# Kernel optimization log

Measured on AMD Instinct MI355X. Metric: run time of the kernel, lower is better.

Reference implementation:

```python
import jax, jax.numpy as jnp
import numpy as np

N = 50000   # nodes
E = 800000  # edges
IN = 128
HID = 128
L = 4       # GraphConv layers
OUT = 47    # classes
EPS = 1e-5  # BatchNorm eps


def setup_inputs() -> dict:
    key = jax.random.key(0)
    ks = jax.random.split(key, 12)
    feat = jax.random.normal(ks[0], (N, IN), jnp.float32)
    src = jax.random.randint(ks[1], (E,), 0, N, jnp.int32)
    dst = jax.random.randint(ks[2], (E,), 0, N, jnp.int32)
    enc_W = jax.random.normal(ks[3], (L, IN, HID), jnp.float32) * 0.05
    enc_bias = jnp.zeros((HID,), jnp.float32)
    bn_gamma = jnp.ones((L, HID), jnp.float32)
    bn_beta = jnp.zeros((L, HID), jnp.float32)
    bn_mean = jax.random.normal(ks[4], (L, HID), jnp.float32) * 0.1
    bn_var = jnp.ones((L, HID), jnp.float32) + 0.1 * jax.random.uniform(ks[5], (L, HID), jnp.float32)
    cls_W0 = jax.random.normal(ks[6], (HID * L, HID), jnp.float32) * 0.05
    cls_b0 = jnp.zeros((HID,), jnp.float32)
    cls_gamma0 = jnp.ones((HID,), jnp.float32)
    cls_beta0 = jnp.zeros((HID,), jnp.float32)
    cls_mean0 = jax.random.normal(ks[7], (HID,), jnp.float32) * 0.1
    cls_var0 = jnp.ones((HID,), jnp.float32) + 0.1 * jax.random.uniform(ks[8], (HID,), jnp.float32)
    cls_W1 = jax.random.normal(ks[9], (HID, OUT), jnp.float32) * 0.05
    cls_b1 = jnp.zeros((OUT,), jnp.float32)
    return dict(feat=feat, src=src, dst=dst, enc_W=enc_W, enc_bias=enc_bias,
                bn_gamma=bn_gamma, bn_beta=bn_beta, bn_mean=bn_mean, bn_var=bn_var,
                cls_W0=cls_W0, cls_b0=cls_b0, cls_gamma0=cls_gamma0, cls_beta0=cls_beta0,
                cls_mean0=cls_mean0, cls_var0=cls_var0, cls_W1=cls_W1, cls_b1=cls_b1)


def _bn_eval(x, gamma, beta, mean, var):
    return (x - mean) * (gamma * jax.lax.rsqrt(var + EPS)) + beta


def reference(feat, src, dst, enc_W, enc_bias, bn_gamma, bn_beta, bn_mean, bn_var,
              cls_W0, cls_b0, cls_gamma0, cls_beta0, cls_mean0, cls_var0, cls_W1, cls_b1):
    ones = jnp.ones((E,), jnp.float32)
    out_deg = jnp.clip(jax.ops.segment_sum(ones, src, num_segments=N), 1.0)
    in_deg = jnp.clip(jax.ops.segment_sum(ones, dst, num_segments=N), 1.0)
    norm_src = jax.lax.rsqrt(out_deg)[:, None]  # [N,1]
    norm_dst = jax.lax.rsqrt(in_deg)[:, None]

    h = feat  # inference: dropout = identity
    feat_lst = []
    for i in range(L):
        # GraphConv 'both': D_out^{-1/2} pre-scale, XW, scatter-add over edges, D_in^{-1/2} post-scale
        hw = (h * norm_src) @ enc_W[i]                         # [N,HID]
        agg = jax.ops.segment_sum(hw[src], dst, num_segments=N)  # sparse neighbor aggregation
        h = agg * norm_dst
        if i == L - 1:  # only last GraphConv has bias
            h = h + enc_bias
        h = _bn_eval(h, bn_gamma[i], bn_beta[i], bn_mean[i], bn_var[i])
        h = jax.nn.relu(h)
        feat_lst.append(h)

    h = jnp.concatenate(feat_lst, axis=-1)  # JK concat -> [N, HID*L]
    # classifier layer 0: Linear + BN + ReLU (dropout off in eval)
    h = _bn_eval(h @ cls_W0 + cls_b0, cls_gamma0, cls_beta0, cls_mean0, cls_var0)
    h = jax.nn.relu(h)
    # classifier layer 1: Linear only
    return h @ cls_W1 + cls_b1  # [N, OUT]
```

## Files before the change

kernel.cpp:

```cpp
#include <hip/hip_runtime.h>
#include <hip/hip_bf16.h>
#include <hip/hip_fp16.h>

#define EPS 1e-5f
#define HB 128
#define HRANGE 25600
#define NN2 51200

typedef __attribute__((ext_vector_type(8))) short short8;
typedef __attribute__((ext_vector_type(4))) float f32x4;

__device__ __forceinline__ unsigned short f2bf_rn(float f) {
    unsigned u = __builtin_bit_cast(unsigned, f);
    u += 0x7fffu + ((u >> 16) & 1u);
    return (unsigned short)(u >> 16);
}
__device__ __forceinline__ float bf2f(unsigned short h) {
    return __builtin_bit_cast(float, (unsigned)h << 16);
}
__device__ __forceinline__ unsigned packsplit(float x) {
    unsigned short h = f2bf_rn(x);
    unsigned short l = f2bf_rn(x - bf2f(h));
    return ((unsigned)h << 16) | l;
}

__global__ __launch_bounds__(1024) void hist_kernel(
    const int* __restrict__ src, const int* __restrict__ dst,
    unsigned* __restrict__ histW, int E, int EperB) {
    __shared__ unsigned cnt[HRANGE];
    const int b = blockIdx.x, tid = threadIdx.x;
    const long e0 = (long)b * EperB;
    const long e1 = min(e0 + (long)EperB, (long)E);
    #pragma unroll 2
    for (int arr = 0; arr < 2; ++arr) {
        const int* a = arr ? src : dst;
        for (int j = tid; j < HRANGE; j += 1024) cnt[j] = 0;
        __syncthreads();
        for (long e = e0 + tid; e < e1; e += 1024) {
            int v = a[e];
            atomicAdd(&cnt[v >> 1], 1u << ((v & 1) << 4));
        }
        __syncthreads();
        unsigned* o = histW + ((size_t)(arr * HB + b)) * HRANGE;
        for (int j = tid; j < HRANGE; j += 1024) o[j] = cnt[j];
        __syncthreads();
    }
}

__global__ __launch_bounds__(256) void merge_kernel(
    const unsigned short* __restrict__ hist16, int* __restrict__ indeg,
    unsigned short* __restrict__ bp16, float* __restrict__ nsrc,
    float* __restrict__ ndst, int N) {
    int n = blockIdx.x * blockDim.x + threadIdx.x;
    if (n >= NN2) return;
    unsigned s = 0;
    #pragma unroll 8
    for (int b = 0; b < HB; ++b) {
        unsigned c = hist16[(size_t)b * NN2 + n];
        bp16[(size_t)b * NN2 + n] = (unsigned short)s;
        s += c;
    }
    unsigned s2 = 0;
    #pragma unroll 8
    for (int b = 0; b < HB; ++b) s2 += hist16[(size_t)(HB + b) * NN2 + n];
    if (n < N) {
        indeg[n] = (int)s;
        ndst[n] = rsqrtf((float)max((int)s, 1));
        nsrc[n] = rsqrtf((float)max((int)s2, 1));
    }
}

__global__ __launch_bounds__(256) void scan_partial_kernel(const int* __restrict__ deg,
                                                           int* __restrict__ bsums, int n) {
    __shared__ int wsum[4];
    const int tid = threadIdx.x, lane = tid & 63, wid = tid >> 6;
    const int i0 = blockIdx.x * 1024 + tid * 4;
    int s = 0;
    if (i0 + 3 < n) {
        int4 v = *(const int4*)(deg + i0);
        s = v.x + v.y + v.z + v.w;
    } else {
        for (int j = 0; j < 4; ++j) if (i0 + j < n) s += deg[i0 + j];
    }
    #pragma unroll
    for (int off = 32; off >= 1; off >>= 1) s += __shfl_down(s, off, 64);
    if (lane == 0) wsum[wid] = s;
    __syncthreads();
    if (tid == 0) bsums[blockIdx.x] = wsum[0] + wsum[1] + wsum[2] + wsum[3];
}

__global__ __launch_bounds__(64) void scan_bsums_kernel(int* __restrict__ bsums,
                                                        int* __restrict__ offs, int nb, int n) {
    int lane = threadIdx.x;
    int v = (lane < nb) ? bsums[lane] : 0;
    int x = v;
    #pragma unroll
    for (int off = 1; off < 64; off <<= 1) {
        int t = __shfl_up(x, off, 64);
        if (lane >= off) x += t;
    }
    if (lane < nb) bsums[lane] = x - v;
    if (lane == 63) offs[n] = x;
}

__global__ __launch_bounds__(256) void scan_final_kernel(const int* __restrict__ deg,
                                                         const int* __restrict__ bsums,
                                                         int* __restrict__ offs, int n) {
    __shared__ int wsum[4];
    const int tid = threadIdx.x, lane = tid & 63, wid = tid >> 6;
    const int i0 = blockIdx.x * 1024 + tid * 4;
    int d0 = 0, d1 = 0, d2 = 0, d3 = 0;
    if (i0 + 3 < n) {
        int4 v = *(const int4*)(deg + i0);
        d0 = v.x; d1 = v.y; d2 = v.z; d3 = v.w;
    } else {
        if (i0 + 0 < n) d0 = deg[i0 + 0];
        if (i0 + 1 < n) d1 = deg[i0 + 1];
        if (i0 + 2 < n) d2 = deg[i0 + 2];
        if (i0 + 3 < n) d3 = deg[i0 + 3];
    }
    int s = d0 + d1 + d2 + d3;
    int x = s;
    #pragma unroll
    for (int off = 1; off < 64; off <<= 1) {
        int t = __shfl_up(x, off, 64);
        if (lane >= off) x += t;
    }
    if (lane == 63) wsum[wid] = x;
    __syncthreads();
    int wpre = 0;
    #pragma unroll
    for (int w = 0; w < 4; ++w) if (w < wid) wpre += wsum[w];
    int base = bsums[blockIdx.x] + wpre + (x - s);
    if (i0 + 0 < n) offs[i0 + 0] = base;
    if (i0 + 1 < n) offs[i0 + 1] = base + d0;
    if (i0 + 2 < n) offs[i0 + 2] = base + d0 + d1;
    if (i0 + 3 < n) offs[i0 + 3] = base + d0 + d1 + d2;
}

__global__ __launch_bounds__(1024) void fill_kernel(
    const int* __restrict__ src, const int* __restrict__ dst,
    const int* __restrict__ offs, const unsigned short* __restrict__ bp16,
    int* __restrict__ csc, int E, int EperB) {
    __shared__ unsigned cur[HRANGE];
    const int b = blockIdx.x, tid = threadIdx.x;
    const long e0 = (long)b * EperB;
    const long e1 = min(e0 + (long)EperB, (long)E);
    for (int j = tid; j < HRANGE; j += 1024) cur[j] = 0;
    __syncthreads();
    const unsigned short* bprow = bp16 + (size_t)b * NN2;
    for (long e = e0 + tid; e < e1; e += 1024) {
        int d = dst[e];
        int sh = (d & 1) << 4;
        unsigned old = atomicAdd(&cur[d >> 1], 1u << sh);
        unsigned rank = (old >> sh) & 0xffffu;
        unsigned p = (unsigned)offs[d] + (unsigned)bprow[d] + rank;
        csc[p] = src[e];
    }
}

__global__ void pack_w_kernel(const float* __restrict__ B, short* __restrict__ hi,
                              short* __restrict__ lo, int K, int NCF,
                              int strideB, int ncols) {
    int t = blockIdx.x * blockDim.x + threadIdx.x;
    int KF = K >> 5;
    int total = NCF * KF * 64;
    if (t >= total) return;
    int lane = t & 63;
    int kf = (t >> 6) % KF;
    int cf = (t >> 6) / KF;
    int col = cf * 16 + (lane & 15);
    int k0 = kf * 32 + (lane >> 4) * 8;
    int o = t * 8;
    #pragma unroll
    for (int j = 0; j < 8; ++j) {
        float x = (col < ncols) ? B[(size_t)(k0 + j) * strideB + col] : 0.f;
        unsigned short h = f2bf_rn(x);
        hi[o + j] = (short)h;
        lo[o + j] = (short)f2bf_rn(x - bf2f(h));
    }
}

template<bool PACKED>
__global__ __launch_bounds__(256) void mfma_gemm_kernel(
    const void* __restrict__ Av, const short* __restrict__ Bhi, const short* __restrict__ Blo,
    const float* __restrict__ nsrc, __half* __restrict__ C, int M) {
    __shared__ short Bh_sh[16384];
    __shared__ short Bl_sh[16384];
    const int tid = threadIdx.x;
    const int lane = tid & 63;
    const int wid  = tid >> 6;
    const int row0 = blockIdx.x * 128 + wid * 32;
    const int rsub = lane & 15;
    const int kg   = lane >> 4;

    short8 ahi[2][4], alo[2][4];
    #pragma unroll
    for (int rf = 0; rf < 2; ++rf) {
        const int rowa = min(row0 + rf * 16 + rsub, M - 1);
        #pragma unroll
        for (int kf = 0; kf < 4; ++kf) {
            short8 h, l;
            if (PACKED) {
                const unsigned* ap = (const unsigned*)Av + (size_t)rowa * 128 + kg * 8;
                uint4 u0 = *(const uint4*)(ap + kf * 32);
                uint4 u1 = *(const uint4*)(ap + kf * 32 + 4);
                unsigned uu[8] = {u0.x, u0.y, u0.z, u0.w, u1.x, u1.y, u1.z, u1.w};
                #pragma unroll
                for (int j = 0; j < 8; ++j) {
                    h[j] = (short)(uu[j] >> 16);
                    l[j] = (short)(uu[j] & 0xffffu);
                }
            } else {
                const float* ap = (const float*)Av + (size_t)rowa * 128 + kg * 8;
                float4 v0 = *(const float4*)(ap + kf * 32);
                float4 v1 = *(const float4*)(ap + kf * 32 + 4);
                float v[8] = {v0.x, v0.y, v0.z, v0.w, v1.x, v1.y, v1.z, v1.w};
                #pragma unroll
                for (int j = 0; j < 8; ++j) {
                    unsigned short hb = f2bf_rn(v[j]);
                    h[j] = (short)hb;
                    l[j] = (short)f2bf_rn(v[j] - bf2f(hb));
                }
            }
            ahi[rf][kf] = h; alo[rf][kf] = l;
        }
    }

    #pragma unroll
    for (int i = 0; i < 8; ++i) {
        int o = (tid + i * 256) * 8;
        *(uint4*)&Bh_sh[o] = *(const uint4*)&Bhi[o];
        *(uint4*)&Bl_sh[o] = *(const uint4*)&Blo[o];
    }
    __syncthreads();

    f32x4 acc[2][8];
    #pragma unroll
    for (int rf = 0; rf < 2; ++rf)
        #pragma unroll
        for (int cf = 0; cf < 8; ++cf) acc[rf][cf] = (f32x4){0.f, 0.f, 0.f, 0.f};

    #pragma unroll
    for (int cf = 0; cf < 8; ++cf) {
        #pragma unroll
        for (int kf = 0; kf < 4; ++kf) {
            int o = ((cf * 4 + kf) * 64 + lane) * 8;
            short8 bh = *(const short8*)&Bh_sh[o];
            short8 bl = *(const short8*)&Bl_sh[o];
            #pragma unroll
            for (int rf = 0; rf < 2; ++rf) {
                acc[rf][cf] = __builtin_amdgcn_mfma_f32_16x16x32_bf16(ahi[rf][kf], bh, acc[rf][cf], 0, 0, 0);
                acc[rf][cf] = __builtin_amdgcn_mfma_f32_16x16x32_bf16(alo[rf][kf], bh, acc[rf][cf], 0, 0, 0);
                acc[rf][cf] = __builtin_amdgcn_mfma_f32_16x16x32_bf16(ahi[rf][kf], bl, acc[rf][cf], 0, 0, 0);
            }
        }
    }

    #pragma unroll
    for (int rf = 0; rf < 2; ++rf)
        #pragma unroll
        for (int r = 0; r < 4; ++r) {
            int row = row0 + rf * 16 + kg * 4 + r;
            if (row < M) {
                float sc = nsrc[row];
                __half* cp = C + (size_t)row * 128 + rsub;
                #pragma unroll
                for (int cf = 0; cf < 8; ++cf) cp[cf * 16] = __float2half(acc[rf][cf][r] * sc);
            }
        }
}

__global__ __launch_bounds__(256) void aggregate_kernel(
    const __half* __restrict__ hw, const int* __restrict__ offs, const int* __restrict__ csc,
    const float* __restrict__ norm_dst, const float* __restrict__ bias,
    const float* __restrict__ gamma, const float* __restrict__ beta,
    const float* __restrict__ mean, const float* __restrict__ var,
    unsigned* __restrict__ hout, int n) {
    const int lane = threadIdx.x & 63;
    const int gw = (blockIdx.x * blockDim.x + threadIdx.x) >> 6;
    const int nw = (gridDim.x * blockDim.x) >> 6;
    const int c = lane * 2;

    const float sc0 = gamma[c] * rsqrtf(var[c] + EPS);
    const float sc1 = gamma[c + 1] * rsqrtf(var[c + 1] + EPS);
    const float mn0 = mean[c], mn1 = mean[c + 1];
    const float bt0 = beta[c], bt1 = beta[c + 1];
    const float bi0 = bias ? bias[c] : 0.f;
    const float bi1 = bias ? bias[c + 1] : 0.f;

    for (int v = gw; v < n; v += nw) {
        int e0 = offs[v], e1 = offs[v + 1];
        float2 acc = make_float2(0.f, 0.f);
        int e = e0;
        for (; e + 4 <= e1; e += 4) {
            int s0 = csc[e], s1 = csc[e + 1], s2 = csc[e + 2], s3 = csc[e + 3];
            float2 p0 = __half22float2(*(const __half2*)(hw + (size_t)s0 * 128 + c));
            float2 p1 = __half22float2(*(const __half2*)(hw + (size_t)s1 * 128 + c));
            float2 p2 = __half22float2(*(const __half2*)(hw + (size_t)s2 * 128 + c));
            float2 p3 = __half22float2(*(const __half2*)(hw + (size_t)s3 * 128 + c));
            acc.x += (p0.x + p1.x) + (p2.x + p3.x);
            acc.y += (p0.y + p1.y) + (p2.y + p3.y);
        }
        for (; e < e1; ++e) {
            int s0 = csc[e];
            float2 p0 = __half22float2(*(const __half2*)(hw + (size_t)s0 * 128 + c));
            acc.x += p0.x; acc.y += p0.y;
        }
        float nd = norm_dst[v];
        float h0 = fmaxf((acc.x * nd + bi0 - mn0) * sc0 + bt0, 0.f);
        float h1 = fmaxf((acc.y * nd + bi1 - mn1) * sc1 + bt1, 0.f);
        uint2 w = make_uint2(packsplit(h0), packsplit(h1));
        *(uint2*)(hout + (size_t)v * 128 + c) = w;
    }
}

__global__ __launch_bounds__(256) void classifier_kernel(
    const unsigned* __restrict__ h1, const unsigned* __restrict__ h2,
    const unsigned* __restrict__ h3, const unsigned* __restrict__ h4,
    const short* __restrict__ Bhi, const short* __restrict__ Blo,
    const short* __restrict__ W1hi, const short* __restrict__ W1lo,
    const float* __restrict__ b0,
    const float* __restrict__ g, const float* __restrict__ bt,
    const float* __restrict__ mn, const float* __restrict__ vr,
    const float* __restrict__ b1,
    float* __restrict__ out, int M) {
    __shared__ short Bh_sh[2][4096];
    __shared__ short Bl_sh[2][4096];
    __shared__ unsigned zw[4][16 * 128];
    const int tid = threadIdx.x, lane = tid & 63, wid = tid >> 6;
    const int rsub = lane & 15;
    const int kg   = lane >> 4;
    const int row0 = blockIdx.x * 128 + wid * 32;
    const unsigned* hb[4] = {h1, h2, h3, h4};

    const int scf = tid >> 5, ssub = tid & 31;
    const int sl = scf * 512 + ssub * 16;

    float biasv[8], scalev[8], meanv[8], betav[8];
    #pragma unroll
    for (int cf = 0; cf < 8; ++cf) {
        int col = cf * 16 + rsub;
        biasv[cf] = b0[col];
        scalev[cf] = g[col] * rsqrtf(vr[col] + EPS);
        meanv[cf] = mn[col];
        betav[cf] = bt[col];
    }

    f32x4 acc[2][8];
    #pragma unroll
    for (int rf = 0; rf < 2; ++rf)
        #pragma unroll
        for (int cf = 0; cf < 8; ++cf) acc[rf][cf] = (f32x4){0.f, 0.f, 0.f, 0.f};

    {
        size_t goff = ((size_t)(scf * 16 + 0) * 64) * 8 + ssub * 16;
        *(uint4*)&Bh_sh[0][sl]     = *(const uint4*)&Bhi[goff];
        *(uint4*)&Bh_sh[0][sl + 8] = *(const uint4*)&Bhi[goff + 8];
        *(uint4*)&Bl_sh[0][sl]     = *(const uint4*)&Blo[goff];
        *(uint4*)&Bl_sh[0][sl + 8] = *(const uint4*)&Blo[goff + 8];
    }
    __syncthreads();

    const int rowa0 = min(row0 + rsub, M - 1);
    const int rowa1 = min(row0 + 16 + rsub, M - 1);

    for (int kf16 = 0; kf16 < 16; ++kf16) {
        const int cur = kf16 & 1;
        uint4 st0, st1, st2, st3;
        if (kf16 < 15) {
            size_t goff = ((size_t)(scf * 16 + kf16 + 1) * 64) * 8 + ssub * 16;
            st0 = *(const uint4*)&Bhi[goff];
            st1 = *(const uint4*)&Bhi[goff + 8];
            st2 = *(const uint4*)&Blo[goff];
            st3 = *(const uint4*)&Blo[goff + 8];
        }
        short8 ah[2], al[2];
        #pragma unroll
        for (int rf = 0; rf < 2; ++rf) {
            const unsigned* ap = hb[kf16 >> 2] + (size_t)(rf ? rowa1 : rowa0) * 128
                                 + (kf16 & 3) * 32 + kg * 8;
            uint4 u0 = *(const uint4*)(ap);
            uint4 u1 = *(const uint4*)(ap + 4);
            unsigned uu[8] = {u0.x, u0.y, u0.z, u0.w, u1.x, u1.y, u1.z, u1.w};
            #pragma unroll
            for (int j = 0; j < 8; ++j) {
                ah[rf][j] = (short)(uu[j] >> 16);
                al[rf][j] = (short)(uu[j] & 0xffffu);
            }
        }
        #pragma unroll
        for (int cf = 0; cf < 8; ++cf) {
            int o = (cf * 64 + lane) * 8;
            short8 bh = *(const short8*)&Bh_sh[cur][o];
            short8 bl = *(const short8*)&Bl_sh[cur][o];
            #pragma unroll
            for (int rf = 0; rf < 2; ++rf) {
                acc[rf][cf] = __builtin_amdgcn_mfma_f32_16x16x32_bf16(ah[rf], bh, acc[rf][cf], 0, 0, 0);
                acc[rf][cf] = __builtin_amdgcn_mfma_f32_16x16x32_bf16(al[rf], bh, acc[rf][cf], 0, 0, 0);
                acc[rf][cf] = __builtin_amdgcn_mfma_f32_16x16x32_bf16(ah[rf], bl, acc[rf][cf], 0, 0, 0);
            }
        }
        if (kf16 < 15) {
            *(uint4*)&Bh_sh[cur ^ 1][sl]     = st0;
            *(uint4*)&Bh_sh[cur ^ 1][sl + 8] = st1;
            *(uint4*)&Bl_sh[cur ^ 1][sl]     = st2;
            *(uint4*)&Bl_sh[cur ^ 1][sl + 8] = st3;
        }
        __syncthreads();
    }

    f32x4 oacc[2][3];
    #pragma unroll
    for (int rf = 0; rf < 2; ++rf)
        #pragma unroll
        for (int cf = 0; cf < 3; ++cf) oacc[rf][cf] = (f32x4){0.f, 0.f, 0.f, 0.f};

    #pragma unroll
    for (int rf = 0; rf < 2; ++rf) {
        #pragma unroll
        for (int cf = 0; cf < 8; ++cf) {
            int col = cf * 16 + rsub;
            #pragma unroll
            for (int r = 0; r < 4; ++r) {
                int rloc = kg * 4 + r;
                float z = fmaxf((acc[rf][cf][r] + biasv[cf] - meanv[cf]) * scalev[cf] + betav[cf], 0.f);
                zw[wid][rloc * 128 + (col ^ ((rloc & 7) << 2))] = packsplit(z);
            }
        }
        const int rloc = rsub;
        const int sw = (rloc & 7) << 2;
        #pragma unroll
        for (int kf = 0; kf < 4; ++kf) {
            int k0 = kf * 32 + kg * 8;
            uint4 ua = *(const uint4*)&zw[wid][rloc * 128 + (k0 ^ sw)];
            uint4 ub = *(const uint4*)&zw[wid][rloc * 128 + ((k0 + 4) ^ sw)];
            unsigned uu[8] = {ua.x, ua.y, ua.z, ua.w, ub.x, ub.y, ub.z, ub.w};
            short8 zh, zl;
            #pragma unroll
            for (int j = 0; j < 8; ++j) {
                zh[j] = (short)(uu[j] >> 16);
                zl[j] = (short)(uu[j] & 0xffffu);
            }
            #pragma unroll
            for (int cf = 0; cf < 3; ++cf) {
                int bidx = ((cf * 4 + kf) * 64 + lane) * 8;
                short8 wh = *(const short8*)(W1hi + bidx);
                short8 wl = *(const short8*)(W1lo + bidx);
                oacc[rf][cf] = __builtin_amdgcn_mfma_f32_16x16x32_bf16(zh, wh, oacc[rf][cf], 0, 0, 0);
                oacc[rf][cf] = __builtin_amdgcn_mfma_f32_16x16x32_bf16(zl, wh, oacc[rf][cf], 0, 0, 0);
                oacc[rf][cf] = __builtin_amdgcn_mfma_f32_16x16x32_bf16(zh, wl, oacc[rf][cf], 0, 0, 0);
            }
        }
    }

    #pragma unroll
    for (int rf = 0; rf < 2; ++rf)
        #pragma unroll
        for (int cf = 0; cf < 3; ++cf) {
            int col = cf * 16 + rsub;
            if (col < 47) {
                float bb = b1[col];
                #pragma unroll
                for (int r = 0; r < 4; ++r) {
                    int row = row0 + rf * 16 + kg * 4 + r;
                    if (row < M) out[(size_t)row * 47 + col] = oacc[rf][cf][r] + bb;
                }
            }
        }
}

extern "C" void kernel_launch(void* const* d_in, const int* in_sizes, int n_in,
                              void* d_out, int out_size, void* d_ws, size_t ws_size,
                              hipStream_t stream) {
    const float* feat     = (const float*)d_in[0];
    const int*   src      = (const int*)d_in[1];
    const int*   dst      = (const int*)d_in[2];
    const float* enc_W    = (const float*)d_in[3];
    const float* enc_bias = (const float*)d_in[4];
    const float* bn_gamma = (const float*)d_in[5];
    const float* bn_beta  = (const float*)d_in[6];
    const float* bn_mean  = (const float*)d_in[7];
    const float* bn_var   = (const float*)d_in[8];
    const float* cls_W0   = (const float*)d_in[9];
    const float* cls_b0   = (const float*)d_in[10];
    const float* cls_g0   = (const float*)d_in[11];
    const float* cls_be0  = (const float*)d_in[12];
    const float* cls_m0   = (const float*)d_in[13];
    const float* cls_v0   = (const float*)d_in[14];
    const float* cls_W1   = (const float*)d_in[15];
    const float* cls_b1   = (const float*)d_in[16];
    float* out = (float*)d_out;

    const int N_ = in_sizes[0] / 128;
    const int E_ = in_sizes[1];

    char* p = (char*)d_ws;
    auto alloc = [&](size_t bytes) {
        char* r = p;
        p += (bytes + 255) & ~(size_t)255;
        return r;
    };
    __half* h_b = (__half*)alloc((size_t)N_ * 128 * 2);
    unsigned* hl[4];
    for (int i = 0; i < 4; ++i) hl[i] = (unsigned*)alloc((size_t)N_ * 128 * 4);
    float* norm_src = (float*)alloc((size_t)NN2 * 4);
    float* norm_dst = (float*)alloc((size_t)NN2 * 4);
    int* indeg  = (int*)alloc((size_t)NN2 * 4);
    int* offs   = (int*)alloc((size_t)(N_ + 1) * 4);
    int* csc    = (int*)alloc((size_t)E_ * 4);
    int* bsums  = (int*)alloc(256 * 4);
    unsigned* histW = (unsigned*)alloc((size_t)2 * HB * HRANGE * 4);
    unsigned short* bp16 = (unsigned short*)alloc((size_t)HB * NN2 * 2);
    short* encBhi = (short*)alloc(4 * 16384 * 2);
    short* encBlo = (short*)alloc(4 * 16384 * 2);
    short* clsBhi = (short*)alloc(65536 * 2);
    short* clsBlo = (short*)alloc(65536 * 2);
    short* w1hi   = (short*)alloc(6144 * 2);
    short* w1lo   = (short*)alloc(6144 * 2);

    const int EperB = (E_ + HB - 1) / HB;
    const int nb = (N_ + 1023) / 1024;

    hist_kernel<<<HB, 1024, 0, stream>>>(src, dst, histW, E_, EperB);
    merge_kernel<<<(NN2 + 255) / 256, 256, 0, stream>>>(
        (const unsigned short*)histW, indeg, bp16, norm_src, norm_dst, N_);
    scan_partial_kernel<<<nb, 256, 0, stream>>>(indeg, bsums, N_);
    scan_bsums_kernel<<<1, 64, 0, stream>>>(bsums, offs, nb, N_);
    scan_final_kernel<<<nb, 256, 0, stream>>>(indeg, bsums, offs, N_);
    fill_kernel<<<HB, 1024, 0, stream>>>(src, dst, offs, bp16, csc, E_, EperB);

    for (int i = 0; i < 4; ++i)
        pack_w_kernel<<<8, 256, 0, stream>>>(enc_W + (size_t)i * 128 * 128,
                                             encBhi + i * 16384, encBlo + i * 16384,
                                             128, 8, 128, 128);
    pack_w_kernel<<<32, 256, 0, stream>>>(cls_W0, clsBhi, clsBlo, 512, 8, 128, 128);
    pack_w_kernel<<<3, 256, 0, stream>>>(cls_W1, w1hi, w1lo, 128, 3, 47, 47);

    const int gblocks = (N_ + 127) / 128;
    const int agg_blocks = (N_ + 3) / 4;

    for (int i = 0; i < 4; ++i) {
        if (i == 0)
            mfma_gemm_kernel<false><<<gblocks, 256, 0, stream>>>(
                feat, encBhi, encBlo, norm_src, h_b, N_);
        else
            mfma_gemm_kernel<true><<<gblocks, 256, 0, stream>>>(
                hl[i - 1], encBhi + i * 16384, encBlo + i * 16384, norm_src, h_b, N_);
        aggregate_kernel<<<agg_blocks, 256, 0, stream>>>(
            h_b, offs, csc, norm_dst,
            (i == 3) ? enc_bias : nullptr,
            bn_gamma + i * 128, bn_beta + i * 128, bn_mean + i * 128, bn_var + i * 128,
            hl[i], N_);
    }
    classifier_kernel<<<gblocks, 256, 0, stream>>>(
        hl[0], hl[1], hl[2], hl[3], clsBhi, clsBlo, w1hi, w1lo, cls_b0,
        cls_g0, cls_be0, cls_m0, cls_v0, cls_b1, out, N_);
}
```

Baseline: 354.6 us.

## Pad CSC rows to multiples of eight with a zero dummy node for vector gathers

Each node's in-degree is rounded up to a multiple of eight when building offsets. The padding slots in the CSC array are prefilled with a sentinel index that points to a zeroed extra row of the hidden buffer. The aggregation loop then reads indices with two int4 loads and gathers eight neighbours per iteration with no scalar tail. This adds wasted gathers on padding entries (average degree is about 16, so roughly a quarter extra), an extra fill kernel and a memset, in exchange for vectorised index loads and a branch-free inner loop.

```diff
diff --git a/kernel.cpp b/kernel.cpp
--- a/kernel.cpp
+++ b/kernel.cpp
@@ -48,7 +48,7 @@
 }
 
 __global__ __launch_bounds__(256) void merge_kernel(
-    const unsigned short* __restrict__ hist16, int* __restrict__ indeg,
+    const unsigned short* __restrict__ hist16, int* __restrict__ pdeg,
     unsigned short* __restrict__ bp16, float* __restrict__ nsrc,
     float* __restrict__ ndst, int N) {
     int n = blockIdx.x * blockDim.x + threadIdx.x;
@@ -64,7 +64,7 @@
     #pragma unroll 8
     for (int b = 0; b < HB; ++b) s2 += hist16[(size_t)(HB + b) * NN2 + n];
     if (n < N) {
-        indeg[n] = (int)s;
+        pdeg[n] = (int)((s + 7u) & ~7u);
         ndst[n] = rsqrtf((float)max((int)s, 1));
         nsrc[n] = rsqrtf((float)max((int)s2, 1));
     }
@@ -136,6 +136,16 @@
     if (i0 + 1 < n) offs[i0 + 1] = base + d0;
     if (i0 + 2 < n) offs[i0 + 2] = base + d0 + d1;
     if (i0 + 3 < n) offs[i0 + 3] = base + d0 + d1 + d2;
+}
+
+__global__ void fill_pad_kernel(int* __restrict__ csc, int total, int N) {
+    int i = blockIdx.x * blockDim.x + threadIdx.x;
+    int o = i * 4;
+    if (o + 3 < total) {
+        *(int4*)(csc + o) = make_int4(N, N, N, N);
+    } else {
+        for (int j = 0; j < 4 && o + j < total; ++j) csc[o + j] = N;
+    }
 }
 
 __global__ __launch_bounds__(1024) void fill_kernel(
@@ -290,22 +300,21 @@
     const float bi1 = bias ? bias[c + 1] : 0.f;
 
     for (int v = gw; v < n; v += nw) {
-        int e0 = offs[v], e1 = offs[v + 1];
+        const int e0 = offs[v], e1 = offs[v + 1];
         float2 acc = make_float2(0.f, 0.f);
-        int e = e0;
-        for (; e + 4 <= e1; e += 4) {
-            int s0 = csc[e], s1 = csc[e + 1], s2 = csc[e + 2], s3 = csc[e + 3];
-            float2 p0 = __half22float2(*(const __half2*)(hw + (size_t)s0 * 128 + c));
-            float2 p1 = __half22float2(*(const __half2*)(hw + (size_t)s1 * 128 + c));
-            float2 p2 = __half22float2(*(const __half2*)(hw + (size_t)s2 * 128 + c));
-            float2 p3 = __half22float2(*(const __half2*)(hw + (size_t)s3 * 128 + c));
-            acc.x += (p0.x + p1.x) + (p2.x + p3.x);
-            acc.y += (p0.y + p1.y) + (p2.y + p3.y);
-        }
-        for (; e < e1; ++e) {
-            int s0 = csc[e];
-            float2 p0 = __half22float2(*(const __half2*)(hw + (size_t)s0 * 128 + c));
-            acc.x += p0.x; acc.y += p0.y;
+        for (int e = e0; e < e1; e += 8) {
+            int4 ca = *(const int4*)(csc + e);
+            int4 cb = *(const int4*)(csc + e + 4);
+            float2 p0 = __half22float2(*(const __half2*)(hw + (size_t)ca.x * 128 + c));
+            float2 p1 = __half22float2(*(const __half2*)(hw + (size_t)ca.y * 128 + c));
+            float2 p2 = __half22float2(*(const __half2*)(hw + (size_t)ca.z * 128 + c));
+            float2 p3 = __half22float2(*(const __half2*)(hw + (size_t)ca.w * 128 + c));
+            float2 p4 = __half22float2(*(const __half2*)(hw + (size_t)cb.x * 128 + c));
+            float2 p5 = __half22float2(*(const __half2*)(hw + (size_t)cb.y * 128 + c));
+            float2 p6 = __half22float2(*(const __half2*)(hw + (size_t)cb.z * 128 + c));
+            float2 p7 = __half22float2(*(const __half2*)(hw + (size_t)cb.w * 128 + c));
+            acc.x += ((p0.x + p1.x) + (p2.x + p3.x)) + ((p4.x + p5.x) + (p6.x + p7.x));
+            acc.y += ((p0.y + p1.y) + (p2.y + p3.y)) + ((p4.y + p5.y) + (p6.y + p7.y));
         }
         float nd = norm_dst[v];
         float h0 = fmaxf((acc.x * nd + bi0 - mn0) * sc0 + bt0, 0.f);
@@ -494,6 +503,7 @@
 
     const int N_ = in_sizes[0] / 128;
     const int E_ = in_sizes[1];
+    const int cscCap = E_ + 7 * N_ + 64;
 
     char* p = (char*)d_ws;
     auto alloc = [&](size_t bytes) {
@@ -501,14 +511,14 @@
         p += (bytes + 255) & ~(size_t)255;
         return r;
     };
-    __half* h_b = (__half*)alloc((size_t)N_ * 128 * 2);
+    __half* h_b = (__half*)alloc((size_t)(N_ + 1) * 128 * 2);
     unsigned* hl[4];
     for (int i = 0; i < 4; ++i) hl[i] = (unsigned*)alloc((size_t)N_ * 128 * 4);
     float* norm_src = (float*)alloc((size_t)NN2 * 4);
     float* norm_dst = (float*)alloc((size_t)NN2 * 4);
-    int* indeg  = (int*)alloc((size_t)NN2 * 4);
+    int* pdeg   = (int*)alloc((size_t)NN2 * 4);
     int* offs   = (int*)alloc((size_t)(N_ + 1) * 4);
-    int* csc    = (int*)alloc((size_t)E_ * 4);
+    int* csc    = (int*)alloc((size_t)cscCap * 4);
     int* bsums  = (int*)alloc(256 * 4);
     unsigned* histW = (unsigned*)alloc((size_t)2 * HB * HRANGE * 4);
     unsigned short* bp16 = (unsigned short*)alloc((size_t)HB * NN2 * 2);
@@ -522,12 +532,15 @@
     const int EperB = (E_ + HB - 1) / HB;
     const int nb = (N_ + 1023) / 1024;
 
+    hipMemsetAsync(h_b + (size_t)N_ * 128, 0, 256, stream);
+
     hist_kernel<<<HB, 1024, 0, stream>>>(src, dst, histW, E_, EperB);
     merge_kernel<<<(NN2 + 255) / 256, 256, 0, stream>>>(
-        (const unsigned short*)histW, indeg, bp16, norm_src, norm_dst, N_);
-    scan_partial_kernel<<<nb, 256, 0, stream>>>(indeg, bsums, N_);
+        (const unsigned short*)histW, pdeg, bp16, norm_src, norm_dst, N_);
+    scan_partial_kernel<<<nb, 256, 0, stream>>>(pdeg, bsums, N_);
     scan_bsums_kernel<<<1, 64, 0, stream>>>(bsums, offs, nb, N_);
-    scan_final_kernel<<<nb, 256, 0, stream>>>(indeg, bsums, offs, N_);
+    scan_final_kernel<<<nb, 256, 0, stream>>>(pdeg, bsums, offs, N_);
+    fill_pad_kernel<<<(cscCap / 4 + 255) / 256, 256, 0, stream>>>(csc, cscCap, N_);
     fill_kernel<<<HB, 1024, 0, stream>>>(src, dst, offs, bp16, csc, E_, EperB);
 
     for (int i = 0; i < 4; ++i)
```

Result: faster. 330.1 us (-6.9%).
